# Optimization experiments

Measured on AMD Instinct MI355X. Metric: run time of the kernel, lower is better.

## Reference

```python
import jax, jax.numpy as jnp
import numpy as np

DIM = 256
HEADS = 8
HEAD_DIM = DIM // HEADS
HIDDEN = DIM * 4


def layer_norm(x, w, b, eps=1e-5):
    m = jnp.mean(x, axis=-1, keepdims=True)
    v = jnp.mean((x - m) ** 2, axis=-1, keepdims=True)
    return (x - m) / jnp.sqrt(v + eps) * w + b


def setup_inputs() -> dict:
    key = jax.random.key(0)
    ks = jax.random.split(key, 12)
    s = lambda fan_in: 1.0 / np.sqrt(fan_in)
    inp = {
        "x0": jax.random.normal(ks[0], (2, 32, 64, DIM), jnp.float32),
        "x1": jax.random.normal(ks[1], (2, 32, 64, DIM), jnp.float32),
        # torch Linear weights stored [out, in], no bias for qk/v/merge
        "qk_w": jax.random.uniform(ks[2], (DIM, DIM), jnp.float32, -s(DIM), s(DIM)),
        "v_w": jax.random.uniform(ks[3], (DIM, DIM), jnp.float32, -s(DIM), s(DIM)),
        "merge_w": jax.random.uniform(ks[4], (DIM, DIM), jnp.float32, -s(DIM), s(DIM)),
        "ln1_w": jnp.ones((DIM,), jnp.float32),
        "ln1_b": jnp.zeros((DIM,), jnp.float32),
        "ln2_w": jnp.ones((DIM,), jnp.float32),
        "ln2_b": jnp.zeros((DIM,), jnp.float32),
        "fc1_w": jax.random.uniform(ks[5], (HIDDEN, 2 * DIM), jnp.float32, -s(2 * DIM), s(2 * DIM)),
        "fc1_b": jnp.zeros((HIDDEN,), jnp.float32),
        "fc2_w": jax.random.uniform(ks[6], (DIM, HIDDEN), jnp.float32, -s(HIDDEN), s(HIDDEN)),
        "fc2_b": jnp.zeros((DIM,), jnp.float32),
        "gamma": jnp.ones((DIM,), jnp.float32),
    }
    return inp


def reference(x0, x1, qk_w, v_w, merge_w, ln1_w, ln1_b, ln2_w, ln2_b,
              fc1_w, fc1_b, fc2_w, fc2_b, gamma):
    N0, L0, WW0, C = x0.shape
    N1, L1, WW1, _ = x1.shape
    x0f = x0.reshape(N0, L0 * WW0, C)
    x1f = x1.reshape(N1, L1 * WW1, C)

    n0 = layer_norm(x0f, ln1_w, ln1_b)
    n1 = layer_norm(x1f, ln1_w, ln1_b)

    def heads(t):  # [N, S, C] -> [N, H, S, Dh]
        N, S, _ = t.shape
        return t.reshape(N, S, HEADS, HEAD_DIM).transpose(0, 2, 1, 3)

    scale = HEAD_DIM ** -0.25  # sqrt of softmax_temp, applied to both sides
    qk0 = heads(n0 @ qk_w.T) * scale
    qk1 = heads(n1 @ qk_w.T) * scale
    v0 = heads(n0 @ v_w.T)
    v1 = heads(n1 @ v_w.T)

    # shared score matrix, reused for both softmax directions
    sim = jnp.einsum('bhld,bhsd->bhls', qk0, qk1)  # [N,H,L,S]
    attn01 = jax.nn.softmax(sim, axis=-1)
    attn10 = jax.nn.softmax(sim, axis=-2)  # == softmax(sim^T, -1)^T

    m0 = jnp.einsum('bhls,bhsd->bhld', attn01, v1)
    m1 = jnp.einsum('bhls,bhld->bhsd', attn10, v0)

    def unheads(t):  # [N,H,S,Dh] -> [N,S,C]
        N, H, S, D = t.shape
        return t.transpose(0, 2, 1, 3).reshape(N, S, H * D)

    m0 = unheads(m0) @ merge_w.T
    m1 = unheads(m1) @ merge_w.T

    def ffn_residual(x, m):
        h = jnp.concatenate([x, m], axis=-1)
        h = jax.nn.gelu(h @ fc1_w.T + fc1_b, approximate=False)
        h = h @ fc2_w.T + fc2_b
        return x + gamma * layer_norm(h, ln2_w, ln2_b)

    y0 = ffn_residual(x0f, m0).reshape(N0, L0, WW0, C)
    y1 = ffn_residual(x1f, m1).reshape(N1, L1, WW1, C)
    return (y0, y1)
```

## Files before the change

### kernel.cpp

```cpp
#include <hip/hip_runtime.h>
#include <hip/hip_bf16.h>
#include <math.h>


typedef float  f32x4  __attribute__((ext_vector_type(4)));
typedef __bf16 bf16x8 __attribute__((ext_vector_type(8)));

#define MFMA16(A, B, C) __builtin_amdgcn_mfma_f32_16x16x32_bf16((A), (B), (C), 0, 0, 0)

static constexpr int   ROWS  = 8192;
static constexpr float QK_SCALE = 0.42044820762685725f;

__device__ inline unsigned short f2b(float f) {
    __hip_bfloat16 h = __float2bfloat16(f);
    union { __hip_bfloat16 h; unsigned short u; } cv;
    cv.h = h;
    return cv.u;
}

__global__ __launch_bounds__(256) void cvt_w_kernel(
    const float* __restrict__ qkw, const float* __restrict__ vw,
    const float* __restrict__ mw,  const float* __restrict__ w1,
    const float* __restrict__ w2,  unsigned short* __restrict__ o)
{
    int i = blockIdx.x * 256 + threadIdx.x;
    float v;
    if      (i <  65536) v = qkw[i];
    else if (i < 131072) v = vw[i - 65536];
    else if (i < 196608) v = mw[i - 131072];
    else if (i < 720896) v = w1[i - 196608];
    else                 v = w2[i - 720896];
    o[i] = f2b(v);
}

__global__ __launch_bounds__(256) void ln_in_kernel(
    const float* __restrict__ x0, const float* __restrict__ x1,
    const float* __restrict__ w,  const float* __restrict__ b,
    unsigned short* __restrict__ nb,
    unsigned short* __restrict__ acat)
{
    const int wid  = threadIdx.x >> 6;
    const int lane = threadIdx.x & 63;
    const int row  = blockIdx.x * 4 + wid;
    const float* xr = (row < 4096) ? (x0 + (size_t)row * 256)
                                   : (x1 + (size_t)(row - 4096) * 256);
    const int c0 = lane * 4;
    const float4 xv = *(const float4*)(xr + c0);
    float s  = (xv.x + xv.y) + (xv.z + xv.w);
    float sq = (xv.x * xv.x + xv.y * xv.y) + (xv.z * xv.z + xv.w * xv.w);
#pragma unroll
    for (int off = 1; off < 64; off <<= 1) {
        s  += __shfl_xor(s,  off);
        sq += __shfl_xor(sq, off);
    }
    const float mean = s * (1.0f / 256.0f);
    const float var  = sq * (1.0f / 256.0f) - mean * mean;
    const float rs   = rsqrtf(var + 1e-5f);
    const float4 wv4 = *(const float4*)(w + c0);
    const float4 bv4 = *(const float4*)(b + c0);
    ushort4 nv;
    nv.x = f2b((xv.x - mean) * rs * wv4.x + bv4.x);
    nv.y = f2b((xv.y - mean) * rs * wv4.y + bv4.y);
    nv.z = f2b((xv.z - mean) * rs * wv4.z + bv4.z);
    nv.w = f2b((xv.w - mean) * rs * wv4.w + bv4.w);
    *(ushort4*)(nb + (size_t)row * 256 + c0) = nv;
    ushort4 xb;
    xb.x = f2b(xv.x); xb.y = f2b(xv.y); xb.z = f2b(xv.z); xb.w = f2b(xv.w);
    *(ushort4*)(acat + (size_t)row * 512 + c0) = xb;
}

template <bool BIAS, bool GELU_, bool OUTB, bool OUTF>
__global__ __launch_bounds__(256) void gemm_bt(
    const unsigned short* __restrict__ A, const unsigned short* __restrict__ W,
    const float* __restrict__ bias,
    unsigned short* __restrict__ outB, int sB, int oB,
    float* __restrict__ outF,
    int K, float alpha)
{
    __shared__ unsigned short As[64 * 72];
    __shared__ unsigned short Ws[64 * 72];
    const int tid  = threadIdx.x;
    const int wid  = tid >> 6;
    const int lane = tid & 63;
    const int ln   = lane & 15;
    const int quad = lane >> 4;
    const int m0 = blockIdx.x * 64, n0 = blockIdx.y * 64;
    f32x4 acc[4] = {{0,0,0,0},{0,0,0,0},{0,0,0,0},{0,0,0,0}};
    const int srow = tid >> 3;
    const int skc  = (tid & 7) * 8;
    const unsigned short* aP0 = A + (size_t)(m0 + srow)      * K + skc;
    const unsigned short* aP1 = A + (size_t)(m0 + srow + 32) * K + skc;
    const unsigned short* wP0 = W + (size_t)(n0 + srow)      * K + skc;
    const unsigned short* wP1 = W + (size_t)(n0 + srow + 32) * K + skc;
    unsigned short* asW0 = As + srow * 72 + skc;
    unsigned short* asW1 = As + (srow + 32) * 72 + skc;
    unsigned short* wsW0 = Ws + srow * 72 + skc;
    unsigned short* wsW1 = Ws + (srow + 32) * 72 + skc;

    for (int k0 = 0; k0 < K; k0 += 64) {
        *(uint4*)asW0 = *(const uint4*)(aP0 + k0);
        *(uint4*)asW1 = *(const uint4*)(aP1 + k0);
        *(uint4*)wsW0 = *(const uint4*)(wP0 + k0);
        *(uint4*)wsW1 = *(const uint4*)(wP1 + k0);
        __syncthreads();
#pragma unroll
        for (int kk = 0; kk < 64; kk += 32) {
            const bf16x8 af = *(const bf16x8*)(As + (wid * 16 + ln) * 72 + kk + quad * 8);
#pragma unroll
            for (int f = 0; f < 4; ++f) {
                const bf16x8 wf = *(const bf16x8*)(Ws + (f * 16 + ln) * 72 + kk + quad * 8);
                acc[f] = MFMA16(wf, af, acc[f]);
            }
        }
        __syncthreads();
    }

    const int rowm = m0 + wid * 16 + ln;
#pragma unroll
    for (int f = 0; f < 4; ++f) {
        const int cb = n0 + f * 16 + quad * 4;
        float vv[4];
#pragma unroll
        for (int r = 0; r < 4; ++r) {
            float t = acc[f][r] * alpha;
            if (BIAS)  t += bias[cb + r];
            if (GELU_) t = 0.5f * t * (1.0f + erff(t * 0.70710678118654752f));
            vv[r] = t;
        }
        if (OUTB) {
            ushort4 o;
            o.x = f2b(vv[0]); o.y = f2b(vv[1]); o.z = f2b(vv[2]); o.w = f2b(vv[3]);
            *(ushort4*)(outB + (size_t)rowm * sB + oB + cb) = o;
        }
        if (OUTF) {
            float4 o = {vv[0], vv[1], vv[2], vv[3]};
            *(float4*)(outF + (size_t)rowm * 256 + cb) = o;
        }
    }
}

__global__ __launch_bounds__(256) void attn_kernel(
    const unsigned short* __restrict__ qk, const unsigned short* __restrict__ v,
    unsigned short* __restrict__ mo)
{
    __shared__ unsigned short Kl[64 * 72];
    __shared__ unsigned short Vt[32 * 72];
    __shared__ unsigned short Pl[4][16 * 72];
    const int tid  = threadIdx.x;
    const int wid  = tid >> 6;
    const int lane = tid & 63;
    const int ln   = lane & 15;
    const int quad = lane >> 4;
    const int dir = blockIdx.z, bh = blockIdx.y;
    const int b = bh >> 3, h = bh & 7;
    const int qbase = b * 2048 + (dir ? 4096 : 0);
    const int kbase = b * 2048 + (dir ? 0 : 4096);
    const int q0 = blockIdx.x * 64;

    const bf16x8 qf =
        *(const bf16x8*)(qk + (size_t)(qbase + q0 + wid * 16 + ln) * 256 + h * 32 + quad * 8);

    f32x4 oacc[2] = {{0,0,0,0},{0,0,0,0}};
    float lpart = 0.0f;
    const f32x4 zf = {0,0,0,0};
    const int srow = tid >> 2;
    const int sc8  = (tid & 3) * 8;

    for (int kt = 0; kt < 32; ++kt) {
        const int kr0 = kbase + kt * 64;
        *(uint4*)(Kl + srow * 72 + sc8) =
            *(const uint4*)(qk + (size_t)(kr0 + srow) * 256 + h * 32 + sc8);
        {
            union { uint4 q; unsigned short u[8]; } vv;
            vv.q = *(const uint4*)(v + (size_t)(kr0 + srow) * 256 + h * 32 + sc8);
#pragma unroll
            for (int j = 0; j < 8; ++j) Vt[(sc8 + j) * 72 + srow] = vv.u[j];
        }
        __syncthreads();

#pragma unroll
        for (int sub = 0; sub < 4; ++sub) {
            const bf16x8 kf = *(const bf16x8*)(Kl + (sub * 16 + ln) * 72 + quad * 8);
            f32x4 s = MFMA16(kf, qf, zf);
            const float e0 = __expf(s[0]), e1 = __expf(s[1]);
            const float e2 = __expf(s[2]), e3 = __expf(s[3]);
            lpart += (e0 + e1) + (e2 + e3);
            ushort4 pb;
            pb.x = f2b(e0); pb.y = f2b(e1); pb.z = f2b(e2); pb.w = f2b(e3);
            *(ushort4*)(&Pl[wid][ln * 72 + sub * 16 + quad * 4]) = pb;
        }
        __syncthreads();

#pragma unroll
        for (int koff = 0; koff < 64; koff += 32) {
            const bf16x8 pf = *(const bf16x8*)(&Pl[wid][ln * 72 + koff + quad * 8]);
#pragma unroll
            for (int dg = 0; dg < 2; ++dg) {
                const bf16x8 vf = *(const bf16x8*)(Vt + (dg * 16 + ln) * 72 + koff + quad * 8);
                oacc[dg] = MFMA16(vf, pf, oacc[dg]);
            }
        }
        __syncthreads();
    }

    lpart += __shfl_xor(lpart, 16);
    lpart += __shfl_xor(lpart, 32);
    const float rinv = 1.0f / lpart;

    const size_t orow = (size_t)(qbase + q0 + wid * 16 + ln) * 256 + h * 32;
#pragma unroll
    for (int dg = 0; dg < 2; ++dg) {
        ushort4 o;
        o.x = f2b(oacc[dg][0] * rinv);
        o.y = f2b(oacc[dg][1] * rinv);
        o.z = f2b(oacc[dg][2] * rinv);
        o.w = f2b(oacc[dg][3] * rinv);
        *(ushort4*)(mo + orow + dg * 16 + quad * 4) = o;
    }
}

__global__ __launch_bounds__(256) void ln_out_kernel(
    const float* __restrict__ x0, const float* __restrict__ x1,
    const float* __restrict__ h2, const float* __restrict__ w,
    const float* __restrict__ b,  const float* __restrict__ gamma,
    float* __restrict__ out)
{
    const int wid  = threadIdx.x >> 6;
    const int lane = threadIdx.x & 63;
    const int row  = blockIdx.x * 4 + wid;
    const int c0 = lane * 4;
    const float4 hv = *(const float4*)(h2 + (size_t)row * 256 + c0);
    float s  = (hv.x + hv.y) + (hv.z + hv.w);
    float sq = (hv.x * hv.x + hv.y * hv.y) + (hv.z * hv.z + hv.w * hv.w);
#pragma unroll
    for (int off = 1; off < 64; off <<= 1) {
        s  += __shfl_xor(s,  off);
        sq += __shfl_xor(sq, off);
    }
    const float mean = s * (1.0f / 256.0f);
    const float var  = sq * (1.0f / 256.0f) - mean * mean;
    const float rs   = rsqrtf(var + 1e-5f);
    const float* xr = (row < 4096) ? (x0 + (size_t)row * 256)
                                   : (x1 + (size_t)(row - 4096) * 256);
    const float4 xv = *(const float4*)(xr + c0);
    const float4 w4 = *(const float4*)(w + c0);
    const float4 b4 = *(const float4*)(b + c0);
    const float4 g4 = *(const float4*)(gamma + c0);
    float4 y;
    y.x = xv.x + g4.x * ((hv.x - mean) * rs * w4.x + b4.x);
    y.y = xv.y + g4.y * ((hv.y - mean) * rs * w4.y + b4.y);
    y.z = xv.z + g4.z * ((hv.z - mean) * rs * w4.z + b4.z);
    y.w = xv.w + g4.w * ((hv.w - mean) * rs * w4.w + b4.w);
    *(float4*)(out + (size_t)row * 256 + c0) = y;
}

extern "C" void kernel_launch(void* const* d_in, const int* in_sizes, int n_in,
                              void* d_out, int out_size, void* d_ws, size_t ws_size,
                              hipStream_t stream) {
    (void)in_sizes; (void)n_in; (void)out_size; (void)ws_size;
    const float* x0      = (const float*)d_in[0];
    const float* x1      = (const float*)d_in[1];
    const float* qk_w    = (const float*)d_in[2];
    const float* v_w     = (const float*)d_in[3];
    const float* merge_w = (const float*)d_in[4];
    const float* ln1_w   = (const float*)d_in[5];
    const float* ln1_b   = (const float*)d_in[6];
    const float* ln2_w   = (const float*)d_in[7];
    const float* ln2_b   = (const float*)d_in[8];
    const float* fc1_w   = (const float*)d_in[9];
    const float* fc1_b   = (const float*)d_in[10];
    const float* fc2_w   = (const float*)d_in[11];
    const float* fc2_b   = (const float*)d_in[12];
    const float* gamma   = (const float*)d_in[13];
    float* out = (float*)d_out;

    unsigned short* nb   = (unsigned short*)d_ws;
    unsigned short* qkb  = nb   + (size_t)ROWS * 256;
    unsigned short* vb   = qkb  + (size_t)ROWS * 256;
    unsigned short* mb   = vb   + (size_t)ROWS * 256;
    unsigned short* acat = mb   + (size_t)ROWS * 256;
    unsigned short* fc1o = acat + (size_t)ROWS * 512;
    float*          h2   = (float*)(fc1o + (size_t)ROWS * 1024);
    unsigned short* wq   = (unsigned short*)(h2 + (size_t)ROWS * 256);
    unsigned short* wv_  = wq  + 65536;
    unsigned short* wm   = wv_ + 65536;
    unsigned short* w1   = wm  + 65536;
    unsigned short* w2   = w1  + 524288;

    cvt_w_kernel<<<3840, 256, 0, stream>>>(qk_w, v_w, merge_w, fc1_w, fc2_w, wq);
    ln_in_kernel<<<2048, 256, 0, stream>>>(x0, x1, ln1_w, ln1_b, nb, acat);

    gemm_bt<false, false, true, false><<<dim3(128, 4), 256, 0, stream>>>(
        nb, wq, nullptr, qkb, 256, 0, nullptr, 256, QK_SCALE);
    gemm_bt<false, false, true, false><<<dim3(128, 4), 256, 0, stream>>>(
        nb, wv_, nullptr, vb, 256, 0, nullptr, 256, 1.0f);

    attn_kernel<<<dim3(32, 16, 2), 256, 0, stream>>>(qkb, vb, mb);

    gemm_bt<false, false, true, false><<<dim3(128, 4), 256, 0, stream>>>(
        mb, wm, nullptr, acat, 512, 256, nullptr, 256, 1.0f);
    gemm_bt<true, true, true, false><<<dim3(128, 16), 256, 0, stream>>>(
        acat, w1, fc1_b, fc1o, 1024, 0, nullptr, 512, 1.0f);
    gemm_bt<true, false, false, true><<<dim3(128, 4), 256, 0, stream>>>(
        fc1o, w2, fc2_b, nullptr, 0, 0, h2, 1024, 1.0f);

    ln_out_kernel<<<2048, 256, 0, stream>>>(x0, x1, h2, ln2_w, ln2_b, gamma, out);
}
```

Measured before the change: 228.5 us.

## Fuse QK/V projections, pre-transpose V, enlarge FFN GEMM tiles and attention key tiles

QK and V projections now run as one GEMM over a concatenated weight, with V written transposed so the attention kernel can load it with vector copies instead of scalar LDS scatter. Attention processes 128 keys per tile and replaces one barrier with a per-wave lgkmcnt wait, since P is private to each wave. The FFN GEMMs use 128x128 tiles with a 4x4 MFMA fragment per wave for more register reuse. Exact erf GELU is replaced by the tanh approximation, which trades a small accuracy change for cheaper math. The transposed V store is strided and uncoalesced, which may cost some write bandwidth.

```diff
diff --git a/kernel.cpp b/kernel.cpp
--- a/kernel.cpp
+++ b/kernel.cpp
@@ -16,6 +16,14 @@
     union { __hip_bfloat16 h; unsigned short u; } cv;
     cv.h = h;
     return cv.u;
+}
+
+__device__ inline float gelu_f(float x) {
+    float z = 0.7978845608028654f * (x + 0.044715f * x * x * x);
+    z = fminf(fmaxf(z, -15.0f), 15.0f);
+    const float e = __expf(-2.0f * z);
+    const float t = (1.0f - e) / (1.0f + e);
+    return 0.5f * x * (1.0f + t);
 }
 
 __global__ __launch_bounds__(256) void cvt_w_kernel(
@@ -69,14 +77,11 @@
     *(ushort4*)(acat + (size_t)row * 512 + c0) = xb;
 }
 
-template <bool BIAS, bool GELU_, bool OUTB, bool OUTF>
-__global__ __launch_bounds__(256) void gemm_bt(
+__global__ __launch_bounds__(256) void gemm_qkv(
     const unsigned short* __restrict__ A, const unsigned short* __restrict__ W,
-    const float* __restrict__ bias,
-    unsigned short* __restrict__ outB, int sB, int oB,
-    float* __restrict__ outF,
-    int K, float alpha)
-{
+    unsigned short* __restrict__ qkb, unsigned short* __restrict__ vtb)
+{
+    constexpr int K = 256;
     __shared__ unsigned short As[64 * 72];
     __shared__ unsigned short Ws[64 * 72];
     const int tid  = threadIdx.x;
@@ -92,16 +97,11 @@
     const unsigned short* aP1 = A + (size_t)(m0 + srow + 32) * K + skc;
     const unsigned short* wP0 = W + (size_t)(n0 + srow)      * K + skc;
     const unsigned short* wP1 = W + (size_t)(n0 + srow + 32) * K + skc;
-    unsigned short* asW0 = As + srow * 72 + skc;
-    unsigned short* asW1 = As + (srow + 32) * 72 + skc;
-    unsigned short* wsW0 = Ws + srow * 72 + skc;
-    unsigned short* wsW1 = Ws + (srow + 32) * 72 + skc;
-
     for (int k0 = 0; k0 < K; k0 += 64) {
-        *(uint4*)asW0 = *(const uint4*)(aP0 + k0);
-        *(uint4*)asW1 = *(const uint4*)(aP1 + k0);
-        *(uint4*)wsW0 = *(const uint4*)(wP0 + k0);
-        *(uint4*)wsW1 = *(const uint4*)(wP1 + k0);
+        *(uint4*)(As + srow * 72 + skc)        = *(const uint4*)(aP0 + k0);
+        *(uint4*)(As + (srow + 32) * 72 + skc) = *(const uint4*)(aP1 + k0);
+        *(uint4*)(Ws + srow * 72 + skc)        = *(const uint4*)(wP0 + k0);
+        *(uint4*)(Ws + (srow + 32) * 72 + skc) = *(const uint4*)(wP1 + k0);
         __syncthreads();
 #pragma unroll
         for (int kk = 0; kk < 64; kk += 32) {
@@ -114,38 +114,159 @@
         }
         __syncthreads();
     }
-
+    const int rowm = m0 + wid * 16 + ln;
+    if (n0 < 256) {
+#pragma unroll
+        for (int f = 0; f < 4; ++f) {
+            const int cb = n0 + f * 16 + quad * 4;
+            ushort4 o;
+            o.x = f2b(acc[f][0] * QK_SCALE); o.y = f2b(acc[f][1] * QK_SCALE);
+            o.z = f2b(acc[f][2] * QK_SCALE); o.w = f2b(acc[f][3] * QK_SCALE);
+            *(ushort4*)(qkb + (size_t)rowm * 256 + cb) = o;
+        }
+    } else {
+#pragma unroll
+        for (int f = 0; f < 4; ++f) {
+            const int cb = (n0 - 256) + f * 16 + quad * 4;
+#pragma unroll
+            for (int r = 0; r < 4; ++r)
+                vtb[(size_t)(cb + r) * 8192 + rowm] = f2b(acc[f][r]);
+        }
+    }
+}
+
+__global__ __launch_bounds__(256) void gemm_merge(
+    const unsigned short* __restrict__ A, const unsigned short* __restrict__ W,
+    unsigned short* __restrict__ outB)
+{
+    constexpr int K = 256;
+    __shared__ unsigned short As[64 * 72];
+    __shared__ unsigned short Ws[64 * 72];
+    const int tid  = threadIdx.x;
+    const int wid  = tid >> 6;
+    const int lane = tid & 63;
+    const int ln   = lane & 15;
+    const int quad = lane >> 4;
+    const int m0 = blockIdx.x * 64, n0 = blockIdx.y * 64;
+    f32x4 acc[4] = {{0,0,0,0},{0,0,0,0},{0,0,0,0},{0,0,0,0}};
+    const int srow = tid >> 3;
+    const int skc  = (tid & 7) * 8;
+    const unsigned short* aP0 = A + (size_t)(m0 + srow)      * K + skc;
+    const unsigned short* aP1 = A + (size_t)(m0 + srow + 32) * K + skc;
+    const unsigned short* wP0 = W + (size_t)(n0 + srow)      * K + skc;
+    const unsigned short* wP1 = W + (size_t)(n0 + srow + 32) * K + skc;
+    for (int k0 = 0; k0 < K; k0 += 64) {
+        *(uint4*)(As + srow * 72 + skc)        = *(const uint4*)(aP0 + k0);
+        *(uint4*)(As + (srow + 32) * 72 + skc) = *(const uint4*)(aP1 + k0);
+        *(uint4*)(Ws + srow * 72 + skc)        = *(const uint4*)(wP0 + k0);
+        *(uint4*)(Ws + (srow + 32) * 72 + skc) = *(const uint4*)(wP1 + k0);
+        __syncthreads();
+#pragma unroll
+        for (int kk = 0; kk < 64; kk += 32) {
+            const bf16x8 af = *(const bf16x8*)(As + (wid * 16 + ln) * 72 + kk + quad * 8);
+#pragma unroll
+            for (int f = 0; f < 4; ++f) {
+                const bf16x8 wf = *(const bf16x8*)(Ws + (f * 16 + ln) * 72 + kk + quad * 8);
+                acc[f] = MFMA16(wf, af, acc[f]);
+            }
+        }
+        __syncthreads();
+    }
     const int rowm = m0 + wid * 16 + ln;
 #pragma unroll
     for (int f = 0; f < 4; ++f) {
         const int cb = n0 + f * 16 + quad * 4;
-        float vv[4];
-#pragma unroll
-        for (int r = 0; r < 4; ++r) {
-            float t = acc[f][r] * alpha;
-            if (BIAS)  t += bias[cb + r];
-            if (GELU_) t = 0.5f * t * (1.0f + erff(t * 0.70710678118654752f));
-            vv[r] = t;
-        }
-        if (OUTB) {
-            ushort4 o;
-            o.x = f2b(vv[0]); o.y = f2b(vv[1]); o.z = f2b(vv[2]); o.w = f2b(vv[3]);
-            *(ushort4*)(outB + (size_t)rowm * sB + oB + cb) = o;
-        }
-        if (OUTF) {
-            float4 o = {vv[0], vv[1], vv[2], vv[3]};
-            *(float4*)(outF + (size_t)rowm * 256 + cb) = o;
+        ushort4 o;
+        o.x = f2b(acc[f][0]); o.y = f2b(acc[f][1]);
+        o.z = f2b(acc[f][2]); o.w = f2b(acc[f][3]);
+        *(ushort4*)(outB + (size_t)rowm * 512 + 256 + cb) = o;
+    }
+}
+
+template <bool GELU_, bool OUTB>
+__global__ __launch_bounds__(256) void gemm128(
+    const unsigned short* __restrict__ A, const unsigned short* __restrict__ W,
+    const float* __restrict__ bias,
+    unsigned short* __restrict__ outB, float* __restrict__ outF,
+    int K, int NS)
+{
+    __shared__ unsigned short As[128 * 72];
+    __shared__ unsigned short Ws[128 * 72];
+    const int tid  = threadIdx.x;
+    const int wid  = tid >> 6;
+    const int lane = tid & 63;
+    const int ln   = lane & 15;
+    const int quad = lane >> 4;
+    const int m0 = blockIdx.x * 128, n0 = blockIdx.y * 128;
+    const int wm = (wid & 1) * 64, wn = (wid >> 1) * 64;
+    f32x4 acc[4][4];
+#pragma unroll
+    for (int f = 0; f < 4; ++f)
+#pragma unroll
+        for (int i = 0; i < 4; ++i) acc[f][i] = (f32x4){0, 0, 0, 0};
+    const int sr = tid >> 2;
+    const int sc = (tid & 3) * 8;
+    for (int k0 = 0; k0 < K; k0 += 64) {
+        const unsigned short* aB = A + (size_t)m0 * K + k0;
+        const unsigned short* wB = W + (size_t)n0 * K + k0;
+        *(uint4*)(As + sr * 72 + sc)             = *(const uint4*)(aB + (size_t)sr * K + sc);
+        *(uint4*)(As + sr * 72 + sc + 32)        = *(const uint4*)(aB + (size_t)sr * K + sc + 32);
+        *(uint4*)(As + (sr + 64) * 72 + sc)      = *(const uint4*)(aB + (size_t)(sr + 64) * K + sc);
+        *(uint4*)(As + (sr + 64) * 72 + sc + 32) = *(const uint4*)(aB + (size_t)(sr + 64) * K + sc + 32);
+        *(uint4*)(Ws + sr * 72 + sc)             = *(const uint4*)(wB + (size_t)sr * K + sc);
+        *(uint4*)(Ws + sr * 72 + sc + 32)        = *(const uint4*)(wB + (size_t)sr * K + sc + 32);
+        *(uint4*)(Ws + (sr + 64) * 72 + sc)      = *(const uint4*)(wB + (size_t)(sr + 64) * K + sc);
+        *(uint4*)(Ws + (sr + 64) * 72 + sc + 32) = *(const uint4*)(wB + (size_t)(sr + 64) * K + sc + 32);
+        __syncthreads();
+#pragma unroll
+        for (int kk = 0; kk < 64; kk += 32) {
+            bf16x8 af[4], wf[4];
+#pragma unroll
+            for (int i = 0; i < 4; ++i)
+                af[i] = *(const bf16x8*)(As + (wm + i * 16 + ln) * 72 + kk + quad * 8);
+#pragma unroll
+            for (int f = 0; f < 4; ++f)
+                wf[f] = *(const bf16x8*)(Ws + (wn + f * 16 + ln) * 72 + kk + quad * 8);
+#pragma unroll
+            for (int f = 0; f < 4; ++f)
+#pragma unroll
+                for (int i = 0; i < 4; ++i)
+                    acc[f][i] = MFMA16(wf[f], af[i], acc[f][i]);
+        }
+        __syncthreads();
+    }
+#pragma unroll
+    for (int f = 0; f < 4; ++f) {
+        const int feat = n0 + wn + f * 16 + quad * 4;
+        const float4 b4 = *(const float4*)(bias + feat);
+#pragma unroll
+        for (int i = 0; i < 4; ++i) {
+            const int token = m0 + wm + i * 16 + ln;
+            float vv[4] = {acc[f][i][0] + b4.x, acc[f][i][1] + b4.y,
+                           acc[f][i][2] + b4.z, acc[f][i][3] + b4.w};
+            if (GELU_) {
+#pragma unroll
+                for (int r = 0; r < 4; ++r) vv[r] = gelu_f(vv[r]);
+            }
+            if (OUTB) {
+                ushort4 o;
+                o.x = f2b(vv[0]); o.y = f2b(vv[1]); o.z = f2b(vv[2]); o.w = f2b(vv[3]);
+                *(ushort4*)(outB + (size_t)token * NS + feat) = o;
+            } else {
+                float4 o = {vv[0], vv[1], vv[2], vv[3]};
+                *(float4*)(outF + (size_t)token * NS + feat) = o;
+            }
         }
     }
 }
 
 __global__ __launch_bounds__(256) void attn_kernel(
-    const unsigned short* __restrict__ qk, const unsigned short* __restrict__ v,
+    const unsigned short* __restrict__ qk, const unsigned short* __restrict__ vtb,
     unsigned short* __restrict__ mo)
 {
-    __shared__ unsigned short Kl[64 * 72];
-    __shared__ unsigned short Vt[32 * 72];
-    __shared__ unsigned short Pl[4][16 * 72];
+    __shared__ unsigned short Kl[128 * 40];
+    __shared__ unsigned short Vt[32 * 136];
+    __shared__ unsigned short Pl[4][16 * 136];
     const int tid  = threadIdx.x;
     const int wid  = tid >> 6;
     const int lane = tid & 63;
@@ -163,40 +284,41 @@
     f32x4 oacc[2] = {{0,0,0,0},{0,0,0,0}};
     float lpart = 0.0f;
     const f32x4 zf = {0,0,0,0};
-    const int srow = tid >> 2;
-    const int sc8  = (tid & 3) * 8;
-
-    for (int kt = 0; kt < 32; ++kt) {
-        const int kr0 = kbase + kt * 64;
-        *(uint4*)(Kl + srow * 72 + sc8) =
-            *(const uint4*)(qk + (size_t)(kr0 + srow) * 256 + h * 32 + sc8);
-        {
-            union { uint4 q; unsigned short u[8]; } vv;
-            vv.q = *(const uint4*)(v + (size_t)(kr0 + srow) * 256 + h * 32 + sc8);
-#pragma unroll
-            for (int j = 0; j < 8; ++j) Vt[(sc8 + j) * 72 + srow] = vv.u[j];
-        }
-        __syncthreads();
-
-#pragma unroll
-        for (int sub = 0; sub < 4; ++sub) {
-            const bf16x8 kf = *(const bf16x8*)(Kl + (sub * 16 + ln) * 72 + quad * 8);
+    const int krow = tid >> 2;
+    const int kc8  = (tid & 3) * 8;
+    const int vd   = tid >> 3;
+    const int vk8  = (tid & 7) * 8;
+    const unsigned short* vRow = vtb + (size_t)(h * 32 + vd) * 8192;
+
+    for (int kt = 0; kt < 16; ++kt) {
+        const int kpos = kbase + kt * 128;
+        *(uint4*)(Kl + krow * 40 + kc8) =
+            *(const uint4*)(qk + (size_t)(kpos + krow) * 256 + h * 32 + kc8);
+        *(uint4*)(Kl + (krow + 64) * 40 + kc8) =
+            *(const uint4*)(qk + (size_t)(kpos + krow + 64) * 256 + h * 32 + kc8);
+        *(uint4*)(Vt + vd * 136 + vk8)      = *(const uint4*)(vRow + kpos + vk8);
+        *(uint4*)(Vt + vd * 136 + vk8 + 64) = *(const uint4*)(vRow + kpos + vk8 + 64);
+        __syncthreads();
+
+#pragma unroll
+        for (int sub = 0; sub < 8; ++sub) {
+            const bf16x8 kf = *(const bf16x8*)(Kl + (sub * 16 + ln) * 40 + quad * 8);
             f32x4 s = MFMA16(kf, qf, zf);
             const float e0 = __expf(s[0]), e1 = __expf(s[1]);
             const float e2 = __expf(s[2]), e3 = __expf(s[3]);
             lpart += (e0 + e1) + (e2 + e3);
             ushort4 pb;
             pb.x = f2b(e0); pb.y = f2b(e1); pb.z = f2b(e2); pb.w = f2b(e3);
-            *(ushort4*)(&Pl[wid][ln * 72 + sub * 16 + quad * 4]) = pb;
-        }
-        __syncthreads();
-
-#pragma unroll
-        for (int koff = 0; koff < 64; koff += 32) {
-            const bf16x8 pf = *(const bf16x8*)(&Pl[wid][ln * 72 + koff + quad * 8]);
+            *(ushort4*)(&Pl[wid][ln * 136 + sub * 16 + quad * 4]) = pb;
+        }
+        asm volatile("s_waitcnt lgkmcnt(0)" ::: "memory");
+
+#pragma unroll
+        for (int koff = 0; koff < 128; koff += 32) {
+            const bf16x8 pf = *(const bf16x8*)(&Pl[wid][ln * 136 + koff + quad * 8]);
 #pragma unroll
             for (int dg = 0; dg < 2; ++dg) {
-                const bf16x8 vf = *(const bf16x8*)(Vt + (dg * 16 + ln) * 72 + koff + quad * 8);
+                const bf16x8 vf = *(const bf16x8*)(Vt + (dg * 16 + ln) * 136 + koff + quad * 8);
                 oacc[dg] = MFMA16(vf, pf, oacc[dg]);
             }
         }
@@ -276,33 +398,29 @@
 
     unsigned short* nb   = (unsigned short*)d_ws;
     unsigned short* qkb  = nb   + (size_t)ROWS * 256;
-    unsigned short* vb   = qkb  + (size_t)ROWS * 256;
-    unsigned short* mb   = vb   + (size_t)ROWS * 256;
+    unsigned short* vtb  = qkb  + (size_t)ROWS * 256;
+    unsigned short* mb   = vtb  + (size_t)ROWS * 256;
     unsigned short* acat = mb   + (size_t)ROWS * 256;
     unsigned short* fc1o = acat + (size_t)ROWS * 512;
     float*          h2   = (float*)(fc1o + (size_t)ROWS * 1024);
-    unsigned short* wq   = (unsigned short*)(h2 + (size_t)ROWS * 256);
-    unsigned short* wv_  = wq  + 65536;
-    unsigned short* wm   = wv_ + 65536;
+    unsigned short* wqv  = (unsigned short*)(h2 + (size_t)ROWS * 256);
+    unsigned short* wm   = wqv + 131072;
     unsigned short* w1   = wm  + 65536;
     unsigned short* w2   = w1  + 524288;
 
-    cvt_w_kernel<<<3840, 256, 0, stream>>>(qk_w, v_w, merge_w, fc1_w, fc2_w, wq);
+    cvt_w_kernel<<<3840, 256, 0, stream>>>(qk_w, v_w, merge_w, fc1_w, fc2_w, wqv);
     ln_in_kernel<<<2048, 256, 0, stream>>>(x0, x1, ln1_w, ln1_b, nb, acat);
 
-    gemm_bt<false, false, true, false><<<dim3(128, 4), 256, 0, stream>>>(
-        nb, wq, nullptr, qkb, 256, 0, nullptr, 256, QK_SCALE);
-    gemm_bt<false, false, true, false><<<dim3(128, 4), 256, 0, stream>>>(
-        nb, wv_, nullptr, vb, 256, 0, nullptr, 256, 1.0f);
-
-    attn_kernel<<<dim3(32, 16, 2), 256, 0, stream>>>(qkb, vb, mb);
-
-    gemm_bt<false, false, true, false><<<dim3(128, 4), 256, 0, stream>>>(
-        mb, wm, nullptr, acat, 512, 256, nullptr, 256, 1.0f);
-    gemm_bt<true, true, true, false><<<dim3(128, 16), 256, 0, stream>>>(
-        acat, w1, fc1_b, fc1o, 1024, 0, nullptr, 512, 1.0f);
-    gemm_bt<true, false, false, true><<<dim3(128, 4), 256, 0, stream>>>(
-        fc1o, w2, fc2_b, nullptr, 0, 0, h2, 1024, 1.0f);
+    gemm_qkv<<<dim3(128, 8), 256, 0, stream>>>(nb, wqv, qkb, vtb);
+
+    attn_kernel<<<dim3(32, 16, 2), 256, 0, stream>>>(qkb, vtb, mb);
+
+    gemm_merge<<<dim3(128, 4), 256, 0, stream>>>(mb, wm, acat);
+
+    gemm128<true, true><<<dim3(64, 8), 256, 0, stream>>>(
+        acat, w1, fc1_b, fc1o, nullptr, 512, 1024);
+    gemm128<false, false><<<dim3(64, 2), 256, 0, stream>>>(
+        fc1o, w2, fc2_b, nullptr, h2, 1024, 256);
 
     ln_out_kernel<<<2048, 256, 0, stream>>>(x0, x1, h2, ln2_w, ln2_b, gamma, out);
 }
```

Result: faster. 191.2 us (-16.3%).
